# Optimization experiments

Hardware: AMD Instinct MI355X
Metric: run time of the kernel (lower is better)

Reference implementation:

```python
import jax, jax.numpy as jnp
import numpy as np

B, S, D = 4, 2048, 1024
H, Dh = 16, 64


def setup_inputs() -> dict:
    key = jax.random.key(0)
    ks = jax.random.split(key, 9)
    s_in = 1.0 / np.sqrt(D)
    inp = {
        "key": jax.random.normal(ks[0], (B, S, D), jnp.float32),
        "value": jax.random.normal(ks[1], (B, S, D), jnp.float32),
        "query": jax.random.normal(ks[2], (B, S, D), jnp.float32),
        # Linear weights stored as [in, out] (math-equivalent to torch W.T)
        "Wq": jax.random.uniform(ks[3], (D, H * Dh), jnp.float32, -s_in, s_in),
        "bq": jax.random.uniform(ks[4], (H * Dh,), jnp.float32, -s_in, s_in),
        "Wk": jax.random.uniform(ks[5], (D, H * Dh), jnp.float32, -s_in, s_in),
        "bk": jax.random.uniform(ks[6], (H * Dh,), jnp.float32, -s_in, s_in),
        "Wv": jax.random.uniform(ks[7], (D, H * Dh), jnp.float32, -s_in, s_in),
        "bv": jax.random.uniform(ks[8], (H * Dh,), jnp.float32, -s_in, s_in),
    }
    return inp


def reference(key, value, query, Wq, bq, Wk, bk, Wv, bv):
    b, s, _ = key.shape
    # projections -> [B, H, S, Dh]
    q = (query @ Wq + bq).reshape(b, s, H, Dh).transpose(0, 2, 1, 3)
    k = (key @ Wk + bk).reshape(b, s, H, Dh).transpose(0, 2, 1, 3)
    v = (value @ Wv + bv).reshape(b, s, H, Dh).transpose(0, 2, 1, 3)
    scores = jnp.einsum("bhqd,bhkd->bhqk", q, k) / np.sqrt(Dh).astype(np.float32)
    p = jax.nn.softmax(scores, axis=-1)
    out = jnp.einsum("bhqk,bhkd->bhqd", p, v)  # [B, H, S, Dh]
    return out.transpose(0, 2, 1, 3).reshape(b, s, H * Dh)
```

## Files before the change

### kernel.cpp

```cpp
#include <hip/hip_runtime.h>

typedef __bf16 bf16;
typedef __bf16 bf16x8 __attribute__((ext_vector_type(8)));
typedef __bf16 bf16x4 __attribute__((ext_vector_type(4)));
typedef _Float16 f16x4 __attribute__((ext_vector_type(4)));
typedef _Float16 f16x8 __attribute__((ext_vector_type(8)));
typedef __fp16 h16x2 __attribute__((ext_vector_type(2)));
typedef float  f32x4  __attribute__((ext_vector_type(4)));
typedef float  f32x16 __attribute__((ext_vector_type(16)));
typedef unsigned int uint2v __attribute__((ext_vector_type(2)));
typedef unsigned int uint4v __attribute__((ext_vector_type(4)));

#define LOG2E 1.44269504088896340736f
#define SCQ (0.125f * LOG2E)

__device__ __forceinline__ void async16(const void* g, void* l) {
  __builtin_amdgcn_global_load_lds(
      (const __attribute__((address_space(1))) unsigned int*)g,
      (__attribute__((address_space(3))) unsigned int*)l, 16, 0, 0);
}

__device__ __forceinline__ f32x4 mfma_bf16(bf16x8 a, bf16x8 b, f32x4 c) {
  return __builtin_amdgcn_mfma_f32_16x16x32_bf16(a, b, c, 0, 0, 0);
}
__device__ __forceinline__ f32x16 mfma32_bf16(bf16x8 a, bf16x8 b, f32x16 c) {
  return __builtin_amdgcn_mfma_f32_32x32x16_bf16(a, b, c, 0, 0, 0);
}
__device__ __forceinline__ f32x16 mfma32x16_f16(f16x8 a, f16x8 b, f32x16 c) {
  return __builtin_amdgcn_mfma_f32_32x32x16_f16(a, b, c, 0, 0, 0);
}

__global__ __launch_bounds__(256) void prep(const float* __restrict__ q,
                                            const float* __restrict__ k,
                                            const float* __restrict__ v,
                                            const float* __restrict__ W0,
                                            const float* __restrict__ W1,
                                            const float* __restrict__ W2,
                                            bf16* __restrict__ actb,
                                            bf16* __restrict__ Wt) {
  __shared__ float t[64 * 69];
  const int z = blockIdx.y, tid = threadIdx.x;
  if (blockIdx.x < 4096) {
    const float* in = z == 0 ? q : (z == 1 ? k : v);
    bf16* o = actb + (size_t)z * 8388608;
    int i = blockIdx.x * 256 + tid;
    const float4* p = (const float4*)in;
    float4 a = p[i * 2], c = p[i * 2 + 1];
    bf16x8 r;
    r[0] = (bf16)a.x; r[1] = (bf16)a.y; r[2] = (bf16)a.z; r[3] = (bf16)a.w;
    r[4] = (bf16)c.x; r[5] = (bf16)c.y; r[6] = (bf16)c.z; r[7] = (bf16)c.w;
    ((bf16x8*)o)[i] = r;
  } else {
    const float* W = z == 0 ? W0 : (z == 1 ? W1 : W2);
    bf16* O = Wt + (size_t)z * (1024 * 1024);
    int lin = blockIdx.x - 4096;
    int k0 = (lin & 15) * 64, n0 = (lin >> 4) * 64;
    int r0 = tid >> 4, c0 = (tid & 15) * 4;
#pragma unroll
    for (int rr = 0; rr < 4; rr++) {
      int kk = r0 + rr * 16;
      float4 vv = *(const float4*)(W + (k0 + kk) * 1024 + n0 + c0);
      t[kk * 69 + c0 + 0] = vv.x; t[kk * 69 + c0 + 1] = vv.y;
      t[kk * 69 + c0 + 2] = vv.z; t[kk * 69 + c0 + 3] = vv.w;
    }
    __syncthreads();
#pragma unroll
    for (int rr = 0; rr < 4; rr++) {
      int n = r0 + rr * 16;
      bf16x4 o;
#pragma unroll
      for (int j = 0; j < 4; j++) o[j] = (bf16)t[(c0 + j) * 69 + n];
      *(bf16x4*)(O + (n0 + n) * 1024 + k0 + c0) = o;
    }
  }
}

__global__ __launch_bounds__(256, 3) void gemm_qkv(const bf16* __restrict__ Act,
                                                   const bf16* __restrict__ Wt,
                                                   const float* __restrict__ b0,
                                                   const float* __restrict__ b1,
                                                   const float* __restrict__ b2,
                                                   bf16* __restrict__ qo,
                                                   bf16* __restrict__ ko,
                                                   _Float16* __restrict__ vf) {
  __shared__ bf16 smem[16384];
  bf16* sA = smem;
  bf16* sB = smem + 8192;
  const int tid = threadIdx.x;
  const int wave = tid >> 6, lane = tid & 63;
  const int quad = lane >> 4, l15 = lane & 15;
  const int z = blockIdx.z;
  const int m0 = blockIdx.x * 128, n0 = blockIdx.y * 128;
  const bf16* A = Act + (size_t)z * 8388608;
  const bf16* Bt = Wt + (size_t)z * 1048576;
  const float* bias = z == 0 ? b0 : (z == 1 ? b1 : b2);

  const bf16* ap[4]; const bf16* bp[4]; int lo[4];
#pragma unroll
  for (int i = 0; i < 4; i++) {
    int g = wave * 256 + i * 64 + lane;
    int row = g >> 3, jl = (g & 7) ^ (row & 7);
    ap[i] = A + (m0 + row) * 1024 + jl * 8;
    bp[i] = Bt + (n0 + row) * 1024 + jl * 8;
    lo[i] = (wave * 256 + i * 64) * 8;
  }
  const int wm = (wave & 1) * 64, wn = (wave >> 1) * 64;
  f32x4 acc[4][4] = {};

  for (int kt = 0; kt < 16; kt++) {
    const int ko_ = kt * 64;
#pragma unroll
    for (int i = 0; i < 4; i++) async16(ap[i] + ko_, sA + lo[i]);
#pragma unroll
    for (int i = 0; i < 4; i++) async16(bp[i] + ko_, sB + lo[i]);
    __syncthreads();
#pragma unroll
    for (int ks = 0; ks < 2; ks++) {
      bf16x8 af[4], bv[4];
#pragma unroll
      for (int mt = 0; mt < 4; mt++) {
        int m = wm + mt * 16 + l15;
        int ph = (ks * 4 + quad) ^ (m & 7);
        af[mt] = *(const bf16x8*)(sA + m * 64 + ph * 8);
      }
#pragma unroll
      for (int nt = 0; nt < 4; nt++) {
        int n = wn + nt * 16 + l15;
        int ph = (ks * 4 + quad) ^ (n & 7);
        bv[nt] = *(const bf16x8*)(sB + n * 64 + ph * 8);
      }
#pragma unroll
      for (int mt = 0; mt < 4; mt++)
#pragma unroll
        for (int nt = 0; nt < 4; nt++)
          acc[mt][nt] = mfma_bf16(af[mt], bv[nt], acc[mt][nt]);
    }
    __syncthreads();
  }

  if (z != 2) {
    bf16* O = z == 0 ? qo : ko;
    const float sc = z == 0 ? SCQ : 1.0f;
#pragma unroll
    for (int nt = 0; nt < 4; nt++) {
      int n = n0 + wn + nt * 16 + l15;
      float bc = bias[n];
#pragma unroll
      for (int mt = 0; mt < 4; mt++)
#pragma unroll
        for (int r = 0; r < 4; r++) {
          int m = m0 + wm + mt * 16 + quad * 4 + r;
          O[m * 1024 + n] = (bf16)((acc[mt][nt][r] + bc) * sc);
        }
    }
  } else {
    const int b = m0 >> 11, s0 = m0 & 2047;
    const int kvb = s0 >> 7;
    const int mtg0 = (wave & 1) * 4;
    const int hl = quad >> 1, jb = (quad & 1) * 4;
#pragma unroll
    for (int nt = 0; nt < 4; nt++) {
      int n = n0 + wn + nt * 16;
      int hh = n >> 6, db = (n >> 5) & 1;
      int lanep = hl * 32 + (n & 31) + l15;
      float bc = bias[n + l15];
#pragma unroll
      for (int mt = 0; mt < 4; mt++) {
        int fi = (mtg0 + mt) * 2 + db;
        f16x4 pk;
#pragma unroll
        for (int r = 0; r < 4; r++) pk[r] = (_Float16)(acc[mt][nt][r] + bc);
        size_t off = ((((size_t)(b * 16 + hh) * 16 + kvb) * 16 + fi) * 512)
                     + lanep * 8 + jb;
        *(f16x4*)(vf + off) = pk;
      }
    }
  }
}

__global__ __launch_bounds__(256, 2) void attn(const bf16* __restrict__ Q,
                                               const bf16* __restrict__ K,
                                               const _Float16* __restrict__ VF,
                                               float* __restrict__ Out) {
  __shared__ bf16 sQ[16384];
  __shared__ bf16 sK0[4096], sK1[4096];
  __shared__ _Float16 sV0[4096], sV1[4096];
  const int tid = threadIdx.x;
  const int wave = tid >> 6, lane = tid & 63;
  const int l31 = lane & 31, hl = lane >> 5;
  const int q0 = blockIdx.x * 256, hh = blockIdx.y, b = blockIdx.z;
  const bf16* Kbase = K + (size_t)(b * 2048) * 1024 + hh * 64;
  const _Float16* Vbase = VF + (size_t)(b * 16 + hh) * 131072;

  const int g0 = tid, g1 = 256 + tid;
  const int r0s = g0 >> 3, j0s = (g0 & 7) ^ (r0s & 7);
  const int r1s = g1 >> 3, j1s = (g1 & 7) ^ (r1s & 7);
  const bf16* kst0 = Kbase + (size_t)r0s * 1024 + j0s * 8;
  const bf16* kst1 = Kbase + (size_t)r1s * 1024 + j1s * 8;

  auto stageKV = [&](int t, bf16* sk, _Float16* sv) {
    async16(kst0 + (size_t)t * 65536, sk + g0 * 8);
    async16(kst1 + (size_t)t * 65536, sk + g1 * 8);
    async16(Vbase + t * 4096 + g0 * 8, sv + g0 * 8);
    async16(Vbase + t * 4096 + g1 * 8, sv + g1 * 8);
  };

#pragma unroll
  for (int i = 0; i < 8; i++) {
    int g = i * 256 + tid;
    int row = g >> 3, jl = (g & 7) ^ (row & 7);
    async16(Q + (size_t)(b * 2048 + q0 + row) * 1024 + hh * 64 + jl * 8, sQ + g * 8);
  }
  stageKV(0, sK0, sV0);
  __syncthreads();

  bf16x8 qf[2][4];
#pragma unroll
  for (int qc = 0; qc < 2; qc++) {
    int rowq = wave * 64 + qc * 32 + l31, rx = rowq & 7;
#pragma unroll
    for (int i = 0; i < 4; i++)
      qf[qc][i] = *(const bf16x8*)(sQ + rowq * 64 + ((2 * i + hl) ^ rx) * 8);
  }

  f32x16 oacc0[2] = {}, oacc1[2] = {};
  float ls0 = 0.f, ls1 = 0.f;

  auto procP = [&](const f32x16& st, float& lsum, f32x16* oq, const f16x8* va) {
    unsigned int dw[8];
    float ps = 0.f;
#pragma unroll
    for (int s = 0; s < 4; s++) {
      float p0 = __builtin_amdgcn_exp2f(st[4 * s + 0]);
      float p1 = __builtin_amdgcn_exp2f(st[4 * s + 1]);
      float p2 = __builtin_amdgcn_exp2f(st[4 * s + 2]);
      float p3 = __builtin_amdgcn_exp2f(st[4 * s + 3]);
      ps += (p0 + p1) + (p2 + p3);
      dw[2 * s]     = __builtin_bit_cast(unsigned int,
                        __builtin_amdgcn_cvt_pkrtz(p0, p1));
      dw[2 * s + 1] = __builtin_bit_cast(unsigned int,
                        __builtin_amdgcn_cvt_pkrtz(p2, p3));
    }
    lsum += ps;
#pragma unroll
    for (int u = 0; u < 2; u++) {
      uint2v rA = __builtin_amdgcn_permlane32_swap(dw[4 * u + 0],
                                                   dw[4 * u + 2], false, false);
      uint2v rB = __builtin_amdgcn_permlane32_swap(dw[4 * u + 1],
                                                   dw[4 * u + 3], false, false);
      uint4v uu;
      uu[0] = rA[0]; uu[1] = rB[0]; uu[2] = rA[1]; uu[3] = rB[1];
      f16x8 pfrag = __builtin_bit_cast(f16x8, uu);
      __builtin_amdgcn_s_setprio(1);
#pragma unroll
      for (int db = 0; db < 2; db++)
        oq[db] = mfma32x16_f16(va[u * 2 + db], pfrag, oq[db]);
      __builtin_amdgcn_s_setprio(0);
    }
  };

  auto computeT = [&](const bf16* sk, const _Float16* sv) {
#pragma unroll
    for (int t32 = 0; t32 < 2; t32++) {
      int rowk = t32 * 32 + l31, rx = rowk & 7;
      const bf16* kr = sk + rowk * 64;
      bf16x8 kf[4];
#pragma unroll
      for (int i = 0; i < 4; i++)
        kf[i] = *(const bf16x8*)(kr + ((2 * i + hl) ^ rx) * 8);
      f32x16 st0 = {}, st1 = {};
      __builtin_amdgcn_s_setprio(1);
#pragma unroll
      for (int i = 0; i < 4; i++) st0 = mfma32_bf16(kf[i], qf[0][i], st0);
#pragma unroll
      for (int i = 0; i < 4; i++) st1 = mfma32_bf16(kf[i], qf[1][i], st1);
      __builtin_amdgcn_s_setprio(0);
      f16x8 va[4];
#pragma unroll
      for (int u = 0; u < 2; u++)
#pragma unroll
        for (int db = 0; db < 2; db++)
          va[u * 2 + db] =
              *(const f16x8*)(sv + ((t32 * 4 + u * 2 + db) * 64 + lane) * 8);
      procP(st0, ls0, oacc0, va);
      procP(st1, ls1, oacc1, va);
    }
  };

#pragma unroll 1
  for (int t = 0; t < 32; t += 2) {
    stageKV(t + 1, sK1, sV1);
    computeT(sK0, sV0);
    __syncthreads();
    if (t + 2 < 32) stageKV(t + 2, sK0, sV0);
    computeT(sK1, sV1);
    __syncthreads();
  }

  ls0 += __shfl_xor(ls0, 32);
  ls1 += __shfl_xor(ls1, 32);
#pragma unroll
  for (int qc = 0; qc < 2; qc++) {
    float inv = 1.f / (qc == 0 ? ls0 : ls1);
    const f32x16* oq = qc == 0 ? oacc0 : oacc1;
    int qrow = b * 2048 + q0 + wave * 64 + qc * 32 + l31;
    float* orow = Out + (size_t)qrow * 1024 + hh * 64;
#pragma unroll
    for (int db = 0; db < 2; db++)
#pragma unroll
      for (int rg = 0; rg < 4; rg++) {
        float4 v;
        v.x = oq[db][4 * rg + 0] * inv;
        v.y = oq[db][4 * rg + 1] * inv;
        v.z = oq[db][4 * rg + 2] * inv;
        v.w = oq[db][4 * rg + 3] * inv;
        *(float4*)(orow + db * 32 + rg * 8 + 4 * hl) = v;
      }
  }
}

extern "C" void kernel_launch(void* const* d_in, const int* in_sizes, int n_in,
                              void* d_out, int out_size, void* d_ws, size_t ws_size,
                              hipStream_t stream) {
  const float* key   = (const float*)d_in[0];
  const float* value = (const float*)d_in[1];
  const float* query = (const float*)d_in[2];
  const float* Wq = (const float*)d_in[3];
  const float* bq = (const float*)d_in[4];
  const float* Wk = (const float*)d_in[5];
  const float* bk = (const float*)d_in[6];
  const float* Wv = (const float*)d_in[7];
  const float* bv = (const float*)d_in[8];
  float* out = (float*)d_out;

  char* ws = (char*)d_ws;
  bf16* actb   = (bf16*)(ws);
  bf16* wt     = (bf16*)(ws + 50331648);
  bf16* qo     = (bf16*)(ws + 56623104);
  bf16* ko     = (bf16*)(ws + 73400320);
  _Float16* vf = (_Float16*)(ws + 90177536);
  (void)in_sizes; (void)n_in; (void)out_size; (void)ws_size;

  prep<<<dim3(4352, 3), 256, 0, stream>>>(query, key, value, Wq, Wk, Wv, actb, wt);
  gemm_qkv<<<dim3(64, 8, 3), 256, 0, stream>>>(actb, wt, bq, bk, bv, qo, ko, vf);
  attn<<<dim3(8, 16, 4), 256, 0, stream>>>(qo, ko, vf, out);
}
```

Before: 289.7 us.

## Fuse fp32-to-bf16 activation conversion into QKV GEMM with double-buffered B tiles

The separate pass that converts the fp32 activations to a bf16 workspace is removed. The QKV GEMM now loads fp32 activation tiles into registers, converts them, and writes bf16 into shared memory. The weight tile now uses a two-slot shared buffer, and the next k-tile of both operands is prefetched while the current one is in MFMA. This avoids a full write and reread of the activation tensors, at the cost of the GEMM reading twice as many activation bytes and one extra barrier per k-step.

```diff
diff --git a/kernel.cpp b/kernel.cpp
--- a/kernel.cpp
+++ b/kernel.cpp
@@ -30,52 +30,38 @@
   return __builtin_amdgcn_mfma_f32_32x32x16_f16(a, b, c, 0, 0, 0);
 }
 
-__global__ __launch_bounds__(256) void prep(const float* __restrict__ q,
-                                            const float* __restrict__ k,
-                                            const float* __restrict__ v,
-                                            const float* __restrict__ W0,
-                                            const float* __restrict__ W1,
-                                            const float* __restrict__ W2,
-                                            bf16* __restrict__ actb,
-                                            bf16* __restrict__ Wt) {
+__global__ __launch_bounds__(256) void prepw(const float* __restrict__ W0,
+                                             const float* __restrict__ W1,
+                                             const float* __restrict__ W2,
+                                             bf16* __restrict__ Wt) {
   __shared__ float t[64 * 69];
   const int z = blockIdx.y, tid = threadIdx.x;
-  if (blockIdx.x < 4096) {
-    const float* in = z == 0 ? q : (z == 1 ? k : v);
-    bf16* o = actb + (size_t)z * 8388608;
-    int i = blockIdx.x * 256 + tid;
-    const float4* p = (const float4*)in;
-    float4 a = p[i * 2], c = p[i * 2 + 1];
-    bf16x8 r;
-    r[0] = (bf16)a.x; r[1] = (bf16)a.y; r[2] = (bf16)a.z; r[3] = (bf16)a.w;
-    r[4] = (bf16)c.x; r[5] = (bf16)c.y; r[6] = (bf16)c.z; r[7] = (bf16)c.w;
-    ((bf16x8*)o)[i] = r;
-  } else {
-    const float* W = z == 0 ? W0 : (z == 1 ? W1 : W2);
-    bf16* O = Wt + (size_t)z * (1024 * 1024);
-    int lin = blockIdx.x - 4096;
-    int k0 = (lin & 15) * 64, n0 = (lin >> 4) * 64;
-    int r0 = tid >> 4, c0 = (tid & 15) * 4;
-#pragma unroll
-    for (int rr = 0; rr < 4; rr++) {
-      int kk = r0 + rr * 16;
-      float4 vv = *(const float4*)(W + (k0 + kk) * 1024 + n0 + c0);
-      t[kk * 69 + c0 + 0] = vv.x; t[kk * 69 + c0 + 1] = vv.y;
-      t[kk * 69 + c0 + 2] = vv.z; t[kk * 69 + c0 + 3] = vv.w;
-    }
-    __syncthreads();
-#pragma unroll
-    for (int rr = 0; rr < 4; rr++) {
-      int n = r0 + rr * 16;
-      bf16x4 o;
-#pragma unroll
-      for (int j = 0; j < 4; j++) o[j] = (bf16)t[(c0 + j) * 69 + n];
-      *(bf16x4*)(O + (n0 + n) * 1024 + k0 + c0) = o;
-    }
-  }
-}
-
-__global__ __launch_bounds__(256, 3) void gemm_qkv(const bf16* __restrict__ Act,
+  const float* W = z == 0 ? W0 : (z == 1 ? W1 : W2);
+  bf16* O = Wt + (size_t)z * (1024 * 1024);
+  int lin = blockIdx.x;
+  int k0 = (lin & 15) * 64, n0 = (lin >> 4) * 64;
+  int r0 = tid >> 4, c0 = (tid & 15) * 4;
+#pragma unroll
+  for (int rr = 0; rr < 4; rr++) {
+    int kk = r0 + rr * 16;
+    float4 vv = *(const float4*)(W + (k0 + kk) * 1024 + n0 + c0);
+    t[kk * 69 + c0 + 0] = vv.x; t[kk * 69 + c0 + 1] = vv.y;
+    t[kk * 69 + c0 + 2] = vv.z; t[kk * 69 + c0 + 3] = vv.w;
+  }
+  __syncthreads();
+#pragma unroll
+  for (int rr = 0; rr < 4; rr++) {
+    int n = r0 + rr * 16;
+    bf16x4 o;
+#pragma unroll
+    for (int j = 0; j < 4; j++) o[j] = (bf16)t[(c0 + j) * 69 + n];
+    *(bf16x4*)(O + (n0 + n) * 1024 + k0 + c0) = o;
+  }
+}
+
+__global__ __launch_bounds__(256, 3) void gemm_qkv(const float* __restrict__ Aq,
+                                                   const float* __restrict__ Ak,
+                                                   const float* __restrict__ Av,
                                                    const bf16* __restrict__ Wt,
                                                    const float* __restrict__ b0,
                                                    const float* __restrict__ b1,
@@ -83,37 +69,67 @@
                                                    bf16* __restrict__ qo,
                                                    bf16* __restrict__ ko,
                                                    _Float16* __restrict__ vf) {
-  __shared__ bf16 smem[16384];
-  bf16* sA = smem;
-  bf16* sB = smem + 8192;
+  __shared__ bf16 sA[8192];
+  __shared__ bf16 sB0[8192], sB1[8192];
   const int tid = threadIdx.x;
   const int wave = tid >> 6, lane = tid & 63;
   const int quad = lane >> 4, l15 = lane & 15;
   const int z = blockIdx.z;
   const int m0 = blockIdx.x * 128, n0 = blockIdx.y * 128;
-  const bf16* A = Act + (size_t)z * 8388608;
+  const float* A = z == 0 ? Aq : (z == 1 ? Ak : Av);
   const bf16* Bt = Wt + (size_t)z * 1048576;
   const float* bias = z == 0 ? b0 : (z == 1 ? b1 : b2);
 
-  const bf16* ap[4]; const bf16* bp[4]; int lo[4];
+  const float* ap[4]; const bf16* bp[4]; int lo[4]; int ga[4];
 #pragma unroll
   for (int i = 0; i < 4; i++) {
     int g = wave * 256 + i * 64 + lane;
     int row = g >> 3, jl = (g & 7) ^ (row & 7);
-    ap[i] = A + (m0 + row) * 1024 + jl * 8;
+    ap[i] = A + (size_t)(m0 + row) * 1024 + jl * 8;
     bp[i] = Bt + (n0 + row) * 1024 + jl * 8;
     lo[i] = (wave * 256 + i * 64) * 8;
+    ga[i] = g * 8;
   }
   const int wm = (wave & 1) * 64, wn = (wave >> 1) * 64;
   f32x4 acc[4][4] = {};
-
+  f32x4 ar[4][2];
+
+  auto loadA = [&](int kt) {
+#pragma unroll
+    for (int i = 0; i < 4; i++) {
+      const float* p = ap[i] + kt * 64;
+      ar[i][0] = *(const f32x4*)(p);
+      ar[i][1] = *(const f32x4*)(p + 4);
+    }
+  };
+  auto writeA = [&]() {
+#pragma unroll
+    for (int i = 0; i < 4; i++) {
+      bf16x8 r;
+#pragma unroll
+      for (int j = 0; j < 4; j++) {
+        r[j]     = (bf16)ar[i][0][j];
+        r[4 + j] = (bf16)ar[i][1][j];
+      }
+      *(bf16x8*)(sA + ga[i]) = r;
+    }
+  };
+
+  loadA(0);
+#pragma unroll
+  for (int i = 0; i < 4; i++) async16(bp[i], sB0 + lo[i]);
+  writeA();
+  __syncthreads();
+
+#pragma unroll 1
   for (int kt = 0; kt < 16; kt++) {
-    const int ko_ = kt * 64;
-#pragma unroll
-    for (int i = 0; i < 4; i++) async16(ap[i] + ko_, sA + lo[i]);
-#pragma unroll
-    for (int i = 0; i < 4; i++) async16(bp[i] + ko_, sB + lo[i]);
-    __syncthreads();
+    bf16* sBc = (kt & 1) ? sB1 : sB0;
+    bf16* sBn = (kt & 1) ? sB0 : sB1;
+    if (kt < 15) {
+#pragma unroll
+      for (int i = 0; i < 4; i++) async16(bp[i] + (kt + 1) * 64, sBn + lo[i]);
+      loadA(kt + 1);
+    }
 #pragma unroll
     for (int ks = 0; ks < 2; ks++) {
       bf16x8 af[4], bv[4];
@@ -127,7 +143,7 @@
       for (int nt = 0; nt < 4; nt++) {
         int n = wn + nt * 16 + l15;
         int ph = (ks * 4 + quad) ^ (n & 7);
-        bv[nt] = *(const bf16x8*)(sB + n * 64 + ph * 8);
+        bv[nt] = *(const bf16x8*)(sBc + n * 64 + ph * 8);
       }
 #pragma unroll
       for (int mt = 0; mt < 4; mt++)
@@ -136,6 +152,10 @@
           acc[mt][nt] = mfma_bf16(af[mt], bv[nt], acc[mt][nt]);
     }
     __syncthreads();
+    if (kt < 15) {
+      writeA();
+      __syncthreads();
+    }
   }
 
   if (z != 2) {
@@ -334,14 +354,14 @@
   float* out = (float*)d_out;
 
   char* ws = (char*)d_ws;
-  bf16* actb   = (bf16*)(ws);
-  bf16* wt     = (bf16*)(ws + 50331648);
-  bf16* qo     = (bf16*)(ws + 56623104);
-  bf16* ko     = (bf16*)(ws + 73400320);
-  _Float16* vf = (_Float16*)(ws + 90177536);
+  bf16* wt     = (bf16*)(ws);
+  bf16* qo     = (bf16*)(ws + 6291456);
+  bf16* ko     = (bf16*)(ws + 23068672);
+  _Float16* vf = (_Float16*)(ws + 39845888);
   (void)in_sizes; (void)n_in; (void)out_size; (void)ws_size;
 
-  prep<<<dim3(4352, 3), 256, 0, stream>>>(query, key, value, Wq, Wk, Wv, actb, wt);
-  gemm_qkv<<<dim3(64, 8, 3), 256, 0, stream>>>(actb, wt, bq, bk, bv, qo, ko, vf);
+  prepw<<<dim3(256, 3), 256, 0, stream>>>(Wq, Wk, Wv, wt);
+  gemm_qkv<<<dim3(64, 8, 3), 256, 0, stream>>>(query, key, value, wt,
+                                               bq, bk, bv, qo, ko, vf);
   attn<<<dim3(8, 16, 4), 256, 0, stream>>>(qo, ko, vf, out);
 }
```

Result: no change. 289.7 us (+0.0%).
